# Kernel optimization log

Hardware: AMD Instinct MI355X
Metric: run time of the kernel (lower is better)

Reference implementation:

```python
import jax, jax.numpy as jnp
import numpy as np

B, T, C = 4, 1024, 1024
H, D = 16, 64


def setup_inputs() -> dict:
    key = jax.random.key(0)
    ks = jax.random.split(key, 5)
    sc = 0.02
    x = jax.random.normal(ks[0], (B, T, C), dtype=jnp.float32)
    Wq = jax.random.normal(ks[1], (H, C, D), dtype=jnp.float32) * sc
    Wk = jax.random.normal(ks[2], (H, C, D), dtype=jnp.float32) * sc
    Wv = jax.random.normal(ks[3], (H, C, D), dtype=jnp.float32) * sc
    Wp = jax.random.normal(ks[4], (H * D, C), dtype=jnp.float32) * sc
    bp = jnp.zeros((C,), dtype=jnp.float32)
    return {"x": x, "Wq": Wq, "Wk": Wk, "Wv": Wv, "Wp": Wp, "bp": bp}


def reference(x, Wq, Wk, Wv, Wp, bp):
    # per-head projections (bias-free, as in nanoGPT Head)
    q = jnp.einsum('btc,hcd->bhtd', x, Wq)
    k = jnp.einsum('btc,hcd->bhtd', x, Wk)
    v = jnp.einsum('btc,hcd->bhtd', x, Wv)
    scale = 1.0 / jnp.sqrt(jnp.asarray(D, dtype=x.dtype))
    scores = jnp.einsum('bhtd,bhsd->bhts', q, k) * scale  # [B,H,T,T]
    causal = jnp.tril(jnp.ones((T, T), dtype=bool))
    scores = jnp.where(causal, scores, jnp.asarray(-jnp.inf, dtype=scores.dtype))
    attn = jax.nn.softmax(scores, axis=-1)
    out = jnp.einsum('bhts,bhsd->bhtd', attn, v)  # [B,H,T,D]
    out = out.transpose(0, 2, 1, 3).reshape(B, T, H * D)  # concat heads
    return out @ Wp + bp  # final projection (dropout=0)
```

## Files before the change

### kernel.cpp

```cpp
#include <hip/hip_runtime.h>
#include <hip/hip_bf16.h>

typedef unsigned short u16;
typedef __bf16 bf16x8 __attribute__((ext_vector_type(8)));
typedef float floatx4 __attribute__((ext_vector_type(4)));

#define SB 4
#define ST 1024
#define SC 1024
#define SH 16
#define SD 64

__device__ __forceinline__ u16 f2bf(float f) {
    unsigned int u = __builtin_bit_cast(unsigned int, f);
    u += 0x7fffu + ((u >> 16) & 1u);
    return (u16)(u >> 16);
}

__device__ __forceinline__ void gload16(const u16* g, u16* l) {
    __builtin_amdgcn_global_load_lds(
        (const __attribute__((address_space(1))) unsigned int*)g,
        (__attribute__((address_space(3))) unsigned int*)l, 16, 0, 0);
}

__global__ void k_prep(const float* __restrict__ x,
                       const float* __restrict__ Wq, const float* __restrict__ Wk,
                       const float* __restrict__ Wv, const float* __restrict__ Wp,
                       u16* __restrict__ xb, u16* __restrict__ Wqkv, u16* __restrict__ Wpt) {
    __shared__ float tile[64 * 65];
    const int id = blockIdx.x, tid = threadIdx.x;
    if (id < 4096) {
        int i = id * 256 + tid;
        float4 v = ((const float4*)x)[i];
        uint2 o;
        o.x = (unsigned)f2bf(v.x) | ((unsigned)f2bf(v.y) << 16);
        o.y = (unsigned)f2bf(v.z) | ((unsigned)f2bf(v.w) << 16);
        ((uint2*)xb)[i] = o;
    } else if (id < 4864) {
        const int id1 = id - 4096;
        const int qkv = id1 >> 8, rem = id1 & 255, h = rem >> 4, c0 = (rem & 15) * 64;
        const float* src = qkv == 0 ? Wq : (qkv == 1 ? Wk : Wv);
        #pragma unroll
        for (int i = 0; i < 16; ++i) {
            int idx = tid + i * 256;
            int r = idx >> 6, d = idx & 63;
            tile[r * 65 + d] = src[(h * SC + c0 + r) * SD + d];
        }
        __syncthreads();
        #pragma unroll
        for (int i = 0; i < 16; ++i) {
            int idx = tid + i * 256;
            int d = idx >> 6, cc = idx & 63;
            Wqkv[(qkv * 1024 + h * SD + d) * SC + c0 + cc] = f2bf(tile[cc * 65 + d]);
        }
    } else {
        const int id2 = id - 4864;
        const int n0 = (id2 & 15) * 64, k0 = (id2 >> 4) * 64;
        #pragma unroll
        for (int i = 0; i < 16; ++i) {
            int idx = tid + i * 256;
            int r = idx >> 6, nn = idx & 63;
            tile[r * 65 + nn] = Wp[(k0 + r) * SC + n0 + nn];
        }
        __syncthreads();
        #pragma unroll
        for (int i = 0; i < 16; ++i) {
            int idx = tid + i * 256;
            int nr = idx >> 6, kk = idx & 63;
            Wpt[(n0 + nr) * (SH * SD) + k0 + kk] = f2bf(tile[kk * 65 + nr]);
        }
    }
}

template<int MODE>
__launch_bounds__(256)
__global__ void k_gemm(const u16* __restrict__ A, const u16* __restrict__ Bt,
                       int M, int N, int K,
                       u16* __restrict__ Qb, u16* __restrict__ Kb, u16* __restrict__ Vt,
                       const float* __restrict__ bias, float* __restrict__ Cout) {
    constexpr int BM = 128, BN = 64, SM = 4, SN = 2;
    __shared__ u16 Als[2][BM * 64];
    __shared__ u16 Bls[2][BN * 64];
    const int tid = threadIdx.x, lane = tid & 63, w = tid >> 6;
    const int quad = lane >> 4, l16 = lane & 15;
    const int sr = lane >> 3, sc = lane & 7;
    const int nt = N / BN;
    const int m0 = (blockIdx.x / nt) * BM, n0 = (blockIdx.x % nt) * BN;
    const int wm = (w >> 1) * 64, wn = (w & 1) * 32;

    auto stage = [&](int buf, int k0) {
        #pragma unroll
        for (int i = 0; i < 4; ++i) {
            int rb = (w * 4 + i) * 8;
            gload16(&A[(long)(m0 + rb + sr) * K + k0 + ((sc ^ sr) << 3)], &Als[buf][rb * 64]);
        }
        #pragma unroll
        for (int i = 0; i < 2; ++i) {
            int rb = (w * 2 + i) * 8;
            gload16(&Bt[(long)(n0 + rb + sr) * K + k0 + ((sc ^ sr) << 3)], &Bls[buf][rb * 64]);
        }
    };

    floatx4 acc[SM][SN] = {};
    const int niter = K / 64;
    stage(0, 0);
    for (int it = 0; it < niter; ++it) {
        const int buf = it & 1;
        __syncthreads();
        if (it + 1 < niter) stage(buf ^ 1, (it + 1) * 64);
        bf16x8 af[SM][2], bfr[SN][2];
        #pragma unroll
        for (int sm = 0; sm < SM; ++sm) {
            int row = wm + sm * 16 + l16;
            #pragma unroll
            for (int ks = 0; ks < 2; ++ks)
                af[sm][ks] = *(const bf16x8*)&Als[buf][row * 64 + (((ks * 4 + quad) ^ (row & 7)) << 3)];
        }
        #pragma unroll
        for (int sn = 0; sn < SN; ++sn) {
            int row = wn + sn * 16 + l16;
            #pragma unroll
            for (int ks = 0; ks < 2; ++ks)
                bfr[sn][ks] = *(const bf16x8*)&Bls[buf][row * 64 + (((ks * 4 + quad) ^ (row & 7)) << 3)];
        }
        #pragma unroll
        for (int ks = 0; ks < 2; ++ks)
            #pragma unroll
            for (int sm = 0; sm < SM; ++sm)
                #pragma unroll
                for (int sn = 0; sn < SN; ++sn)
                    acc[sm][sn] = __builtin_amdgcn_mfma_f32_16x16x32_bf16(bfr[sn][ks], af[sm][ks], acc[sm][sn], 0, 0, 0);
    }
    if (MODE == 0) {
        const int qkv = n0 >> 10, h = (n0 & 1023) >> 6;
        const float qs = qkv == 0 ? 0.18033688011112042f : 1.0f;
        #pragma unroll
        for (int sm = 0; sm < SM; ++sm) {
            const int m = m0 + wm + sm * 16 + l16;
            const int bb = m >> 10, t = m & 1023;
            #pragma unroll
            for (int sn = 0; sn < SN; ++sn) {
                const int d0 = wn + sn * 16 + (quad << 2);
                u16 pk[4];
                #pragma unroll
                for (int r = 0; r < 4; ++r) pk[r] = f2bf(acc[sm][sn][r] * qs);
                if (qkv == 2) {
                    const long vb = (long)(bb * SH + h) * SD * ST + t;
                    #pragma unroll
                    for (int r = 0; r < 4; ++r) Vt[vb + (long)(d0 + r) * ST] = pk[r];
                } else {
                    u16* dst = qkv == 0 ? Qb : Kb;
                    *(uint2*)&dst[(((long)(bb * SH + h) * ST + t) << 6) + d0] = *(uint2*)pk;
                }
            }
        }
    } else {
        #pragma unroll
        for (int sn = 0; sn < SN; ++sn) {
            const int nb = n0 + wn + sn * 16 + (quad << 2);
            const float4 bv = *(const float4*)&bias[nb];
            #pragma unroll
            for (int sm = 0; sm < SM; ++sm) {
                const int m = m0 + wm + sm * 16 + l16;
                float4 o;
                o.x = acc[sm][sn][0] + bv.x;
                o.y = acc[sm][sn][1] + bv.y;
                o.z = acc[sm][sn][2] + bv.z;
                o.w = acc[sm][sn][3] + bv.w;
                *(float4*)&Cout[(long)m * N + nb] = o;
            }
        }
    }
}

__launch_bounds__(256)
__global__ void k_attn(const u16* __restrict__ Qg, const u16* __restrict__ Kg,
                       const u16* __restrict__ Vtg, u16* __restrict__ Og) {
    __shared__ u16 Kls[2][64 * 64];
    __shared__ u16 Vls[2][64 * 64];
    __shared__ u16 Pls[64 * 64];
    const int tid = threadIdx.x, lane = tid & 63, w = tid >> 6;
    const int quad = lane >> 4, l16 = lane & 15;
    const int sr = lane >> 3, sc = lane & 7;
    const int tile = 15 - (blockIdx.x >> 6);
    const int bh = blockIdx.x & 63;
    const int t0 = tile * 64;
    const int b = bh >> 4, h = bh & 15;
    const u16* Qbh = Qg + (long)bh * ST * SD;
    const u16* Kbh = Kg + (long)bh * ST * SD;
    const u16* Vbh = Vtg + (long)bh * SD * ST;

    bf16x8 qf[2];
    {
        const u16* qrow = Qbh + (t0 + w * 16 + l16) * SD;
        qf[0] = *(const bf16x8*)&qrow[quad * 8];
        qf[1] = *(const bf16x8*)&qrow[32 + quad * 8];
    }
    floatx4 oacc[4] = {};
    float lsum = 0.f;
    const int myt = t0 + w * 16 + l16;
    const int rowP = w * 16 + l16;

    auto stage = [&](int buf, int s0) {
        #pragma unroll
        for (int i = 0; i < 2; ++i) {
            int rb = (w * 2 + i) * 8;
            gload16(&Kbh[(s0 + rb + sr) * SD + ((sc ^ sr) << 3)], &Kls[buf][rb * 64]);
            gload16(&Vbh[(rb + sr) * ST + s0 + ((sc ^ sr) << 3)], &Vls[buf][rb * 64]);
        }
    };

    stage(0, 0);
    for (int j = 0; j <= tile; ++j) {
        const int buf = j & 1;
        const int s0 = j * 64;
        __syncthreads();
        if (j < tile) stage(buf ^ 1, s0 + 64);

        floatx4 sa[4] = {};
        #pragma unroll
        for (int sn = 0; sn < 4; ++sn) {
            int row = sn * 16 + l16;
            #pragma unroll
            for (int ks = 0; ks < 2; ++ks) {
                bf16x8 kf = *(const bf16x8*)&Kls[buf][row * 64 + (((ks * 4 + quad) ^ (row & 7)) << 3)];
                sa[sn] = __builtin_amdgcn_mfma_f32_16x16x32_bf16(kf, qf[ks], sa[sn], 0, 0, 0);
            }
        }
        const bool diag = (j == tile);
        #pragma unroll
        for (int sn = 0; sn < 4; ++sn) {
            const int sl = sn * 16 + (quad << 2);
            u16 pk[4];
            #pragma unroll
            for (int r = 0; r < 4; ++r) {
                float e = __builtin_exp2f(sa[sn][r]);
                if (diag && s0 + sl + r > myt) e = 0.f;
                lsum += e;
                pk[r] = (u16)(__builtin_bit_cast(unsigned int, e) >> 16);
            }
            *(uint2*)&Pls[rowP * 64 + (((sl >> 3) ^ (rowP & 7)) << 3) + ((quad & 1) << 2)] = *(uint2*)pk;
        }
        bf16x8 pf[2];
        #pragma unroll
        for (int ks = 0; ks < 2; ++ks)
            pf[ks] = *(const bf16x8*)&Pls[rowP * 64 + (((ks * 4 + quad) ^ (rowP & 7)) << 3)];
        #pragma unroll
        for (int dn = 0; dn < 4; ++dn) {
            int row = dn * 16 + l16;
            #pragma unroll
            for (int ks = 0; ks < 2; ++ks) {
                bf16x8 vf = *(const bf16x8*)&Vls[buf][row * 64 + (((ks * 4 + quad) ^ (row & 7)) << 3)];
                oacc[dn] = __builtin_amdgcn_mfma_f32_16x16x32_bf16(vf, pf[ks], oacc[dn], 0, 0, 0);
            }
        }
    }
    float l = lsum;
    l += __shfl_xor(l, 16);
    l += __shfl_xor(l, 32);
    const float inv = 1.0f / l;
    const long obase = ((long)(b * ST + myt) << 10) + h * SD;
    #pragma unroll
    for (int dn = 0; dn < 4; ++dn) {
        u16 pk[4];
        #pragma unroll
        for (int r = 0; r < 4; ++r) pk[r] = f2bf(oacc[dn][r] * inv);
        *(uint2*)&Og[obase + dn * 16 + (quad << 2)] = *(uint2*)pk;
    }
}

extern "C" void kernel_launch(void* const* d_in, const int* in_sizes, int n_in,
                              void* d_out, int out_size, void* d_ws, size_t ws_size,
                              hipStream_t stream) {
    const float* x  = (const float*)d_in[0];
    const float* Wq = (const float*)d_in[1];
    const float* Wk = (const float*)d_in[2];
    const float* Wv = (const float*)d_in[3];
    const float* Wp = (const float*)d_in[4];
    const float* bp = (const float*)d_in[5];
    float* out = (float*)d_out;

    char* ws = (char*)d_ws;
    u16* xb   = (u16*)(ws);
    u16* Wqkv = (u16*)(ws + (8ll  << 20));
    u16* Wpt  = (u16*)(ws + (14ll << 20));
    u16* Qb   = (u16*)(ws + (16ll << 20));
    u16* Kb   = (u16*)(ws + (24ll << 20));
    u16* Vt   = (u16*)(ws + (32ll << 20));
    u16* Ob   = (u16*)(ws + (40ll << 20));

    k_prep<<<5120, 256, 0, stream>>>(x, Wq, Wk, Wv, Wp, xb, Wqkv, Wpt);
    k_gemm<0><<<32 * 48, 256, 0, stream>>>(xb, Wqkv, 4096, 3072, 1024, Qb, Kb, Vt, nullptr, nullptr);
    k_attn<<<1024, 256, 0, stream>>>(Qb, Kb, Vt, Ob);
    k_gemm<1><<<32 * 16, 256, 0, stream>>>(Ob, Wpt, 4096, 1024, 1024, nullptr, nullptr, nullptr, bp, out);
}
```

Measured before the change: 164.2 us.

## Load attention K/V fragments directly from global; use smaller M tile for output GEMM

The attention kernel drops its shared-memory double buffer for K and V. Each wave now loads its MFMA fragments straight from global memory into registers, prefetching the next K block and removing the per-iteration barrier. Separately, the GEMM template gains a BM parameter so the output projection runs with 64-row tiles and twice as many blocks, for better CU fill. The risks are redundant global and cache traffic, since all four waves load the same K/V, plus more register pressure and exposed load latency for V.

```diff
diff --git a/kernel.cpp b/kernel.cpp
--- a/kernel.cpp
+++ b/kernel.cpp
@@ -72,13 +72,13 @@
     }
 }
 
-template<int MODE>
+template<int BM, int MODE>
 __launch_bounds__(256)
 __global__ void k_gemm(const u16* __restrict__ A, const u16* __restrict__ Bt,
                        int M, int N, int K,
                        u16* __restrict__ Qb, u16* __restrict__ Kb, u16* __restrict__ Vt,
                        const float* __restrict__ bias, float* __restrict__ Cout) {
-    constexpr int BM = 128, BN = 64, SM = 4, SN = 2;
+    constexpr int BN = 64, SM = BM / 32, SN = 2;
     __shared__ u16 Als[2][BM * 64];
     __shared__ u16 Bls[2][BN * 64];
     const int tid = threadIdx.x, lane = tid & 63, w = tid >> 6;
@@ -86,12 +86,12 @@
     const int sr = lane >> 3, sc = lane & 7;
     const int nt = N / BN;
     const int m0 = (blockIdx.x / nt) * BM, n0 = (blockIdx.x % nt) * BN;
-    const int wm = (w >> 1) * 64, wn = (w & 1) * 32;
+    const int wm = (w >> 1) * (BM / 2), wn = (w & 1) * 32;
 
     auto stage = [&](int buf, int k0) {
         #pragma unroll
-        for (int i = 0; i < 4; ++i) {
-            int rb = (w * 4 + i) * 8;
+        for (int i = 0; i < BM / 32; ++i) {
+            int rb = (w * (BM / 32) + i) * 8;
             gload16(&A[(long)(m0 + rb + sr) * K + k0 + ((sc ^ sr) << 3)], &Als[buf][rb * 64]);
         }
         #pragma unroll
@@ -176,12 +176,9 @@
 __launch_bounds__(256)
 __global__ void k_attn(const u16* __restrict__ Qg, const u16* __restrict__ Kg,
                        const u16* __restrict__ Vtg, u16* __restrict__ Og) {
-    __shared__ u16 Kls[2][64 * 64];
-    __shared__ u16 Vls[2][64 * 64];
     __shared__ u16 Pls[64 * 64];
     const int tid = threadIdx.x, lane = tid & 63, w = tid >> 6;
     const int quad = lane >> 4, l16 = lane & 15;
-    const int sr = lane >> 3, sc = lane & 7;
     const int tile = 15 - (blockIdx.x >> 6);
     const int bh = blockIdx.x & 63;
     const int t0 = tile * 64;
@@ -201,31 +198,36 @@
     const int myt = t0 + w * 16 + l16;
     const int rowP = w * 16 + l16;
 
-    auto stage = [&](int buf, int s0) {
-        #pragma unroll
-        for (int i = 0; i < 2; ++i) {
-            int rb = (w * 2 + i) * 8;
-            gload16(&Kbh[(s0 + rb + sr) * SD + ((sc ^ sr) << 3)], &Kls[buf][rb * 64]);
-            gload16(&Vbh[(rb + sr) * ST + s0 + ((sc ^ sr) << 3)], &Vls[buf][rb * 64]);
-        }
-    };
-
-    stage(0, 0);
+    const u16* kbase = Kbh + (long)l16 * SD + quad * 8;
+    const u16* vbase = Vbh + (long)l16 * ST + quad * 8;
+
+    bf16x8 kf[4][2];
+    #pragma unroll
+    for (int sn = 0; sn < 4; ++sn)
+        #pragma unroll
+        for (int ks = 0; ks < 2; ++ks)
+            kf[sn][ks] = *(const bf16x8*)&kbase[(long)sn * 16 * SD + ks * 32];
+
     for (int j = 0; j <= tile; ++j) {
-        const int buf = j & 1;
         const int s0 = j * 64;
-        __syncthreads();
-        if (j < tile) stage(buf ^ 1, s0 + 64);
-
         floatx4 sa[4] = {};
         #pragma unroll
         for (int sn = 0; sn < 4; ++sn) {
-            int row = sn * 16 + l16;
-            #pragma unroll
-            for (int ks = 0; ks < 2; ++ks) {
-                bf16x8 kf = *(const bf16x8*)&Kls[buf][row * 64 + (((ks * 4 + quad) ^ (row & 7)) << 3)];
-                sa[sn] = __builtin_amdgcn_mfma_f32_16x16x32_bf16(kf, qf[ks], sa[sn], 0, 0, 0);
-            }
+            sa[sn] = __builtin_amdgcn_mfma_f32_16x16x32_bf16(kf[sn][0], qf[0], sa[sn], 0, 0, 0);
+            sa[sn] = __builtin_amdgcn_mfma_f32_16x16x32_bf16(kf[sn][1], qf[1], sa[sn], 0, 0, 0);
+        }
+        bf16x8 vf[4][2];
+        #pragma unroll
+        for (int dn = 0; dn < 4; ++dn)
+            #pragma unroll
+            for (int ks = 0; ks < 2; ++ks)
+                vf[dn][ks] = *(const bf16x8*)&vbase[(long)dn * 16 * ST + s0 + ks * 32];
+        if (j < tile) {
+            #pragma unroll
+            for (int sn = 0; sn < 4; ++sn)
+                #pragma unroll
+                for (int ks = 0; ks < 2; ++ks)
+                    kf[sn][ks] = *(const bf16x8*)&kbase[(long)(s0 + 64 + sn * 16) * SD + ks * 32];
         }
         const bool diag = (j == tile);
         #pragma unroll
@@ -247,12 +249,8 @@
             pf[ks] = *(const bf16x8*)&Pls[rowP * 64 + (((ks * 4 + quad) ^ (rowP & 7)) << 3)];
         #pragma unroll
         for (int dn = 0; dn < 4; ++dn) {
-            int row = dn * 16 + l16;
-            #pragma unroll
-            for (int ks = 0; ks < 2; ++ks) {
-                bf16x8 vf = *(const bf16x8*)&Vls[buf][row * 64 + (((ks * 4 + quad) ^ (row & 7)) << 3)];
-                oacc[dn] = __builtin_amdgcn_mfma_f32_16x16x32_bf16(vf, pf[ks], oacc[dn], 0, 0, 0);
-            }
+            oacc[dn] = __builtin_amdgcn_mfma_f32_16x16x32_bf16(vf[dn][0], pf[0], oacc[dn], 0, 0, 0);
+            oacc[dn] = __builtin_amdgcn_mfma_f32_16x16x32_bf16(vf[dn][1], pf[1], oacc[dn], 0, 0, 0);
         }
     }
     float l = lsum;
@@ -290,7 +288,7 @@
     u16* Ob   = (u16*)(ws + (40ll << 20));
 
     k_prep<<<5120, 256, 0, stream>>>(x, Wq, Wk, Wv, Wp, xb, Wqkv, Wpt);
-    k_gemm<0><<<32 * 48, 256, 0, stream>>>(xb, Wqkv, 4096, 3072, 1024, Qb, Kb, Vt, nullptr, nullptr);
+    k_gemm<128, 0><<<32 * 48, 256, 0, stream>>>(xb, Wqkv, 4096, 3072, 1024, Qb, Kb, Vt, nullptr, nullptr);
     k_attn<<<1024, 256, 0, stream>>>(Qb, Kb, Vt, Ob);
-    k_gemm<1><<<32 * 16, 256, 0, stream>>>(Ob, Wpt, 4096, 1024, 1024, nullptr, nullptr, nullptr, bp, out);
-}
+    k_gemm<64, 1><<<64 * 16, 256, 0, stream>>>(Ob, Wpt, 4096, 1024, 1024, nullptr, nullptr, nullptr, bp, out);
+}
```

Result: slower. 205.6 us (+25.2%).
